# Optimization experiments

Measured on AMD Instinct MI355X. Metric: run time of the kernel, lower is better.

Reference implementation:

```python
import jax, jax.numpy as jnp
import numpy as np

B = 2048

def _conv(x, w, b, stride):
    y = jax.lax.conv_general_dilated(x, w, (stride, stride), 'VALID',
                                     dimension_numbers=('NCHW', 'OIHW', 'NCHW'))
    return y + b[None, :, None, None]

def _local_conv(x, w, b):
    # w: (Ho, Wo, Co, Ci, kh, kw), b: (Ho, Wo, Co); stride 1, valid
    Ho, Wo, Co, Ci, kh, kw = w.shape
    # patches: (B, Ci, kh*kw, Ho, Wo) -- sliding windows, small fixed loop over kernel taps
    patches = jnp.stack([x[:, :, i:i + Ho, j:j + Wo]
                         for i in range(kh) for j in range(kw)], axis=2)
    wf = w.reshape(Ho, Wo, Co, Ci, kh * kw)
    y = jnp.einsum('bcphw,hwocp->bohw', patches, wf)
    return y + jnp.transpose(b, (2, 0, 1))[None]

def setup_inputs() -> dict:
    key = jax.random.key(0)
    ks = jax.random.split(key, 18)
    s = 0.05
    inp = {
        'x': jax.random.normal(ks[0], (B, 5, 60, 60), dtype=jnp.float32),
        'info': jax.random.normal(ks[1], (B, 8), dtype=jnp.float32),
        'w1': jax.random.normal(ks[2], (32, 5, 3, 3), dtype=jnp.float32) * s,
        'b1': jnp.zeros((32,), dtype=jnp.float32),
        'w2a': jax.random.normal(ks[3], (64, 32, 3, 3), dtype=jnp.float32) * s,
        'b2a': jnp.zeros((64,), dtype=jnp.float32),
        'w2b': jax.random.normal(ks[4], (64, 64, 3, 3), dtype=jnp.float32) * s,
        'b2b': jnp.zeros((64,), dtype=jnp.float32),
        'lw3': jax.random.normal(ks[5], (9, 9, 64, 64, 5, 5), dtype=jnp.float32) * s,
        'lb3': jnp.zeros((9, 9, 64), dtype=jnp.float32),
        'lw4': jax.random.normal(ks[6], (5, 5, 64, 64, 5, 5), dtype=jnp.float32) * s,
        'lb4': jnp.zeros((5, 5, 64), dtype=jnp.float32),
        'lw5': jax.random.normal(ks[7], (3, 3, 64, 64, 3, 3), dtype=jnp.float32) * s,
        'lb5': jnp.zeros((3, 3, 64), dtype=jnp.float32),
        'hw': jax.random.normal(ks[8], (2, 584), dtype=jnp.float32) * s,
        'hb': jnp.zeros((2,), dtype=jnp.float32),
    }
    return inp

def reference(x, info, w1, b1, w2a, b2a, w2b, b2b, lw3, lb3, lw4, lb4, lw5, lb5, hw, hb):
    h = jnp.tanh(_conv(x, w1, b1, 2))            # (B,32,29,29)
    h = jnp.tanh(_conv(h, w2a, b2a, 1))          # (B,64,27,27)
    h = jnp.tanh(_conv(h, w2b, b2b, 2))          # (B,64,13,13)
    h = jnp.tanh(_local_conv(h, lw3, lb3))       # (B,64,9,9)
    h = jnp.tanh(_local_conv(h, lw4, lb4))       # (B,64,5,5)
    h = jnp.tanh(_local_conv(h, lw5, lb5))       # (B,64,3,3)
    h = h.reshape(h.shape[0], -1)                # (B,576)
    h = jnp.concatenate([h, info], axis=1)       # (B,584)
    logits = h @ hw.T + hb                       # (B,2)
    return jax.nn.softmax(logits, axis=1)
```

## Files before the change

kernel.cpp:

```cpp
#include <hip/hip_runtime.h>
#include <stdint.h>

#define THREADS 256

typedef short bf16x8 __attribute__((ext_vector_type(8)));
typedef float f32x4 __attribute__((ext_vector_type(4)));
typedef unsigned uint2_ __attribute__((ext_vector_type(2)));
typedef unsigned short ushort4_ __attribute__((ext_vector_type(4)));

#define GPTR(x) ((const __attribute__((address_space(1))) void*)(x))
#define LPTR(x) ((__attribute__((address_space(3))) void*)(x))

__device__ __forceinline__ unsigned short f2bf(float v) {
  unsigned u = __builtin_bit_cast(unsigned, v);
  u = (u + 0x7fff + ((u >> 16) & 1)) >> 16;
  return (unsigned short)u;
}
__device__ __forceinline__ float bf2f(unsigned short h) {
  return __builtin_bit_cast(float, (unsigned)h << 16);
}
__device__ __forceinline__ float fast_tanh(float x) {
  return 1.f - 2.f / (__expf(2.f * x) + 1.f);
}

__global__ void pack_w1t(const float* __restrict__ w1, float* __restrict__ w1t) {
  int idx = blockIdx.x * THREADS + threadIdx.x;
  if (idx >= 45 * 32) return;
  int t = idx >> 5, co = idx & 31;
  w1t[t * 32 + co] = w1[co * 45 + t];
}

__global__ void __launch_bounds__(256) conv1_direct(
    const float* __restrict__ x, const float* __restrict__ w1t,
    const float* __restrict__ bias, unsigned short* __restrict__ out, int Bc,
    int bstart) {
  constexpr int CI = 5, CO = 32, IH = 60, IW = 60, OH = 29, OW = 29;
  constexpr int RPB = 2, NRB = 15;

  __shared__ float xs[CI * 5 * 60];

  const int tid = threadIdx.x;
  const int b = blockIdx.x / NRB;
  const int qb = blockIdx.x % NRB;
  const int oh0 = qb * RPB;
  const int rows = min(RPB, OH - oh0);
  const int ih0 = oh0 * 2;
  const int ihn = rows * 2 + 1;

  const float* xp = x + (size_t)(bstart + b) * (CI * IH * IW);

  const int nf4 = CI * ihn * 15;
  for (int i = tid; i < nf4; i += 256) {
    int col = i % 15;
    int row = i / 15;
    int ci = row / ihn, r = row % ihn;
    ((float4*)xs)[row * 15 + col] = ((const float4*)xp)[(ci * IH + ih0 + r) * 15 + col];
  }
  __syncthreads();

  const int lane = tid & 63;
  const int wu = __builtin_amdgcn_readfirstlane(tid >> 6);
  if (lane >= rows * OW) return;
  const int r = lane / OW, c = lane % OW;
  const int base = (r * 2) * 60 + c * 2;
  const int cstr = ihn * 60;

  float acc[8];
#pragma unroll
  for (int j = 0; j < 8; j++) acc[j] = bias[wu * 8 + j];

#pragma unroll
  for (int ci = 0; ci < CI; ci++)
#pragma unroll
    for (int kh = 0; kh < 3; kh++)
#pragma unroll
      for (int kw = 0; kw < 3; kw++) {
        const float v = xs[ci * cstr + base + kh * 60 + kw];
        const float* wt = w1t + ((ci * 3 + kh) * 3 + kw) * 32 + wu * 8;
#pragma unroll
        for (int j = 0; j < 8; j++) acc[j] = fmaf(v, wt[j], acc[j]);
      }

  const int p = (oh0 + r) * OW + c;
  bf16x8 o;
#pragma unroll
  for (int j = 0; j < 8; j++) o[j] = (short)f2bf(fast_tanh(acc[j]));
  *(bf16x8*)(out + ((size_t)p * Bc + b) * CO + wu * 8) = o;
}

template <int CI, int KS>
__global__ void __launch_bounds__(THREADS) pack_w(const float* __restrict__ w,
                                                  unsigned short* __restrict__ wp,
                                                  int npos) {
  constexpr int K = CI * KS * KS;
  constexpr int S = K / 32;
  int idx = blockIdx.x * THREADS + threadIdx.x;
  int total = npos * S * 2048;
  if (idx >= total) return;
  int e = idx & 7;
  int lane = (idx >> 3) & 63;
  int mt = (idx >> 9) & 3;
  int rest = idx >> 11;
  int s = rest % S, pos = rest / S;
  int co = mt * 16 + (lane & 15);
  int k = s * 32 + (lane >> 4) * 8 + e;
  int tap = k / CI, ci = k % CI;
  int kh = tap / KS, kw = tap % KS;
  float v = w[((((size_t)pos * 64 + co) * CI + ci) * KS + kh) * KS + kw];
  wp[idx] = f2bf(v);
}

template <int CI, int IH, int IW, int OH, int OW, int KS, int ST, bool LOCAL, int BT>
__global__ void __launch_bounds__(256) conv_mfma(
    const unsigned short* __restrict__ X, const unsigned short* __restrict__ Wp,
    const float* __restrict__ bias, unsigned short* __restrict__ Y, int Bc) {
  constexpr int S = CI * KS * KS / 32;
  constexpr int NPOS = OH * OW;
  constexpr int BW = BT / 64;
  constexpr int CW = 4 / BW;
  constexpr int MT = 4 / CW;

  __shared__ unsigned short aT[2][2048];

  const int tid = threadIdx.x;
  const int lane = tid & 63;
  const int wu = tid >> 6;
  const int n = lane & 15, g = lane >> 4;
  const int bw = wu % BW, cw = wu / BW;

  int wg = blockIdx.x;
  {
    const int nwg = gridDim.x;
    const int q = nwg >> 3, rr = nwg & 7;
    const int xcd = wg & 7, l = wg >> 3;
    wg = (xcd < rr ? xcd * (q + 1) : rr * (q + 1) + (xcd - rr) * q) + l;
  }
  const int pos = wg % NPOS;
  const int btile = wg / NPOS;
  const int oh = pos / OW, ow = pos % OW;
  const int b0 = btile * BT + bw * 64;

  const unsigned short* Wpp = Wp + (LOCAL ? (size_t)pos * (S * 2048) : 0);

  f32x4 acc[MT][4] = {};

  const int bA = b0 + n;

  __builtin_amdgcn_global_load_lds(GPTR(Wpp + tid * 8), LPTR(&aT[0][tid * 8]), 16, 0, 0);

  int buf = 0;
  for (int s = 0; s < S; s++) {
    __syncthreads();
    if (s + 1 < S)
      __builtin_amdgcn_global_load_lds(GPTR(Wpp + (s + 1) * 2048 + tid * 8),
                                       LPTR(&aT[buf ^ 1][tid * 8]), 16, 0, 0);

    const int tap = (s * 32) / CI;
    const int ci0 = (s * 32) % CI + g * 8;
    const int kh = tap / KS, kw = tap % KS;
    const int pin = (oh * ST + kh) * IW + (ow * ST + kw);
    const unsigned short* xb = X + ((size_t)pin * Bc + bA) * CI + ci0;

    bf16x8 bfr[4];
#pragma unroll
    for (int j = 0; j < 4; j++) bfr[j] = *(const bf16x8*)(xb + j * 16 * CI);

    bf16x8 af[MT];
#pragma unroll
    for (int mt = 0; mt < MT; mt++)
      af[mt] = *(const bf16x8*)(&aT[buf][((cw * MT + mt) * 64 + lane) * 8]);

#pragma unroll
    for (int mt = 0; mt < MT; mt++)
#pragma unroll
      for (int j = 0; j < 4; j++)
        acc[mt][j] =
            __builtin_amdgcn_mfma_f32_16x16x32_bf16(af[mt], bfr[j], acc[mt][j], 0, 0, 0);
    buf ^= 1;
  }

#pragma unroll
  for (int mt = 0; mt < MT; mt++) {
#pragma unroll
    for (int j = 0; j < 4; j++) {
      unsigned short o[4];
#pragma unroll
      for (int r = 0; r < 4; r++) {
        const int co = (cw * MT + mt) * 16 + g * 4 + r;
        const float bv = LOCAL ? bias[pos * 64 + co] : bias[co];
        o[r] = f2bf(fast_tanh(acc[mt][j][r] + bv));
      }
      const int b = b0 + j * 16 + n;
      uint2_ pk;
      pk[0] = (unsigned)o[0] | ((unsigned)o[1] << 16);
      pk[1] = (unsigned)o[2] | ((unsigned)o[3] << 16);
      *(uint2_*)(Y + ((size_t)pos * Bc + b) * 64 + (cw * MT + mt) * 16 + g * 4) = pk;
    }
  }
}

__global__ void head_k(const unsigned short* __restrict__ h5,
                       const float* __restrict__ info, const float* __restrict__ hw,
                       const float* __restrict__ hb, float* __restrict__ out, int Bc,
                       int bstart) {
  int b = blockIdx.x * THREADS + threadIdx.x;
  if (b >= Bc) return;
  float l0 = hb[0], l1 = hb[1];
  for (int pos = 0; pos < 9; pos++) {
#pragma unroll
    for (int cb = 0; cb < 8; cb++) {
      bf16x8 v8 = *(const bf16x8*)(h5 + ((size_t)pos * Bc + b) * 64 + cb * 8);
#pragma unroll
      for (int j = 0; j < 8; j++) {
        float v = bf2f((unsigned short)v8[j]);
        int f = (cb * 8 + j) * 9 + pos;
        l0 = fmaf(v, hw[f], l0);
        l1 = fmaf(v, hw[584 + f], l1);
      }
    }
  }
#pragma unroll
  for (int k = 0; k < 8; k++) {
    float v = info[(size_t)(bstart + b) * 8 + k];
    l0 = fmaf(v, hw[576 + k], l0);
    l1 = fmaf(v, hw[584 + 576 + k], l1);
  }
  float m = fmaxf(l0, l1);
  float e0 = __expf(l0 - m), e1 = __expf(l1 - m);
  float s = e0 + e1;
  out[(size_t)(bstart + b) * 2 + 0] = e0 / s;
  out[(size_t)(bstart + b) * 2 + 1] = e1 / s;
}


extern "C" void kernel_launch(void* const* d_in, const int* in_sizes, int n_in,
                              void* d_out, int out_size, void* d_ws, size_t ws_size,
                              hipStream_t stream) {
  const float* x = (const float*)d_in[0];
  const float* info = (const float*)d_in[1];
  const float* w1 = (const float*)d_in[2];
  const float* b1 = (const float*)d_in[3];
  const float* w2a = (const float*)d_in[4];
  const float* b2a = (const float*)d_in[5];
  const float* w2b = (const float*)d_in[6];
  const float* b2b = (const float*)d_in[7];
  const float* lw3 = (const float*)d_in[8];
  const float* lb3 = (const float*)d_in[9];
  const float* lw4 = (const float*)d_in[10];
  const float* lb4 = (const float*)d_in[11];
  const float* lw5 = (const float*)d_in[12];
  const float* lb5 = (const float*)d_in[13];
  const float* hw = (const float*)d_in[14];
  const float* hb = (const float*)d_in[15];
  float* out = (float*)d_out;

  const int B = in_sizes[0] / 18000;

  const size_t SZ2A = 9ull * 2048, SZ2B = 18ull * 2048, SZ3 = 81ull * 50 * 2048,
               SZ4 = 25ull * 50 * 2048, SZ5 = 9ull * 18 * 2048;
  unsigned short* wp2a = (unsigned short*)d_ws;
  unsigned short* wp2b = wp2a + SZ2A;
  unsigned short* wp3 = wp2b + SZ2B;
  unsigned short* wp4 = wp3 + SZ3;
  unsigned short* wp5 = wp4 + SZ4;
  size_t wp_bytes = (SZ2A + SZ2B + SZ3 + SZ4 + SZ5) * 2;
  wp_bytes = (wp_bytes + 255) & ~(size_t)255;
  float* w1t = (float*)((char*)d_ws + wp_bytes);
  size_t w1t_bytes = ((45 * 32 * 4) + 255) & ~(size_t)255;

  const size_t per_sample = 53824 + 93312;
  int Bc = B;
  while (Bc > 256 && wp_bytes + w1t_bytes + (size_t)Bc * per_sample + 4096 > ws_size)
    Bc >>= 1;

  unsigned short* bufA = (unsigned short*)((char*)d_ws + wp_bytes + w1t_bytes);
  unsigned short* bufB =
      (unsigned short*)((char*)d_ws + wp_bytes + w1t_bytes + (size_t)Bc * 53824);

  hipLaunchKernelGGL(pack_w1t, dim3(6), dim3(THREADS), 0, stream, w1, w1t);
  hipLaunchKernelGGL((pack_w<32, 3>), dim3((SZ2A + 255) / 256), dim3(THREADS), 0, stream,
                     w2a, wp2a, 1);
  hipLaunchKernelGGL((pack_w<64, 3>), dim3((SZ2B + 255) / 256), dim3(THREADS), 0, stream,
                     w2b, wp2b, 1);
  hipLaunchKernelGGL((pack_w<64, 5>), dim3((SZ3 + 255) / 256), dim3(THREADS), 0, stream,
                     lw3, wp3, 81);
  hipLaunchKernelGGL((pack_w<64, 5>), dim3((SZ4 + 255) / 256), dim3(THREADS), 0, stream,
                     lw4, wp4, 25);
  hipLaunchKernelGGL((pack_w<64, 3>), dim3((SZ5 + 255) / 256), dim3(THREADS), 0, stream,
                     lw5, wp5, 9);

  const int nchunks = B / Bc;
  for (int c = 0; c < nchunks; c++) {
    const int bstart = c * Bc;

    hipLaunchKernelGGL(conv1_direct, dim3(Bc * 15), dim3(256), 0, stream, x, w1t, b1,
                       bufA, Bc, bstart);
    hipLaunchKernelGGL((conv_mfma<32, 29, 29, 27, 27, 3, 1, false, 256>),
                       dim3(729 * (Bc / 256)), dim3(256), 0, stream, bufA, wp2a, b2a,
                       bufB, Bc);
    hipLaunchKernelGGL((conv_mfma<64, 27, 27, 13, 13, 3, 2, false, 256>),
                       dim3(169 * (Bc / 256)), dim3(256), 0, stream, bufB, wp2b, b2b,
                       bufA, Bc);
    hipLaunchKernelGGL((conv_mfma<64, 13, 13, 9, 9, 5, 1, true, 256>),
                       dim3(81 * (Bc / 256)), dim3(256), 0, stream, bufA, wp3, lb3, bufB,
                       Bc);
    hipLaunchKernelGGL((conv_mfma<64, 9, 9, 5, 5, 5, 1, true, 128>),
                       dim3(25 * (Bc / 128)), dim3(256), 0, stream, bufB, wp4, lb4, bufA,
                       Bc);
    hipLaunchKernelGGL((conv_mfma<64, 5, 5, 3, 3, 3, 1, true, 64>),
                       dim3(9 * (Bc / 64)), dim3(256), 0, stream, bufA, wp5, lb5, bufB,
                       Bc);
    hipLaunchKernelGGL(head_k, dim3((Bc + THREADS - 1) / THREADS), dim3(THREADS), 0,
                       stream, bufB, info, hw, hb, out, Bc, bstart);
  }
}
```

Measured before the change: 567.0 us.

## Preload full conv weights into LDS, read local-conv weights directly from global

For the shared-weight convolutions, each block now loads the entire packed weight tensor into dynamic LDS once, up front, instead of double-buffering one slice per K-step. This removes the per-iteration barrier. The locally-connected layers skip LDS and have each wave read its weight fragments straight from global memory, and the K loop is unrolled by two. The batch chunk is also capped at 1024, which changes the number of passes and the working-set size. The risks are larger LDS use (up to 72KB), which may lower occupancy, and uncoalesced or redundant global weight reads in the local layers.

```diff
diff --git a/kernel.cpp b/kernel.cpp
--- a/kernel.cpp
+++ b/kernel.cpp
@@ -120,7 +120,7 @@
   constexpr int CW = 4 / BW;
   constexpr int MT = 4 / CW;
 
-  __shared__ unsigned short aT[2][2048];
+  extern __shared__ unsigned short wlds[];
 
   const int tid = threadIdx.x;
   const int lane = tid & 63;
@@ -142,19 +142,18 @@
 
   const unsigned short* Wpp = Wp + (LOCAL ? (size_t)pos * (S * 2048) : 0);
 
+  if (!LOCAL) {
+    for (int i = tid; i < S * 256; i += 256)
+      __builtin_amdgcn_global_load_lds(GPTR(Wpp + (size_t)i * 8),
+                                       LPTR(wlds + (size_t)i * 8), 16, 0, 0);
+    __syncthreads();
+  }
+
   f32x4 acc[MT][4] = {};
-
   const int bA = b0 + n;
 
-  __builtin_amdgcn_global_load_lds(GPTR(Wpp + tid * 8), LPTR(&aT[0][tid * 8]), 16, 0, 0);
-
-  int buf = 0;
+#pragma unroll 2
   for (int s = 0; s < S; s++) {
-    __syncthreads();
-    if (s + 1 < S)
-      __builtin_amdgcn_global_load_lds(GPTR(Wpp + (s + 1) * 2048 + tid * 8),
-                                       LPTR(&aT[buf ^ 1][tid * 8]), 16, 0, 0);
-
     const int tap = (s * 32) / CI;
     const int ci0 = (s * 32) % CI + g * 8;
     const int kh = tap / KS, kw = tap % KS;
@@ -167,8 +166,13 @@
 
     bf16x8 af[MT];
 #pragma unroll
-    for (int mt = 0; mt < MT; mt++)
-      af[mt] = *(const bf16x8*)(&aT[buf][((cw * MT + mt) * 64 + lane) * 8]);
+    for (int mt = 0; mt < MT; mt++) {
+      const int t = cw * MT + mt;
+      if (LOCAL)
+        af[mt] = *(const bf16x8*)(Wpp + ((size_t)((s * 4 + t) * 64 + lane) << 3));
+      else
+        af[mt] = *(const bf16x8*)(wlds + ((size_t)((s * 4 + t) * 64 + lane) << 3));
+    }
 
 #pragma unroll
     for (int mt = 0; mt < MT; mt++)
@@ -176,7 +180,6 @@
       for (int j = 0; j < 4; j++)
         acc[mt][j] =
             __builtin_amdgcn_mfma_f32_16x16x32_bf16(af[mt], bfr[j], acc[mt][j], 0, 0, 0);
-    buf ^= 1;
   }
 
 #pragma unroll
@@ -270,6 +273,7 @@
 
   const size_t per_sample = 53824 + 93312;
   int Bc = B;
+  if (Bc > 1024) Bc = 1024;
   while (Bc > 256 && wp_bytes + w1t_bytes + (size_t)Bc * per_sample + 4096 > ws_size)
     Bc >>= 1;
 
@@ -296,11 +300,11 @@
     hipLaunchKernelGGL(conv1_direct, dim3(Bc * 15), dim3(256), 0, stream, x, w1t, b1,
                        bufA, Bc, bstart);
     hipLaunchKernelGGL((conv_mfma<32, 29, 29, 27, 27, 3, 1, false, 256>),
-                       dim3(729 * (Bc / 256)), dim3(256), 0, stream, bufA, wp2a, b2a,
-                       bufB, Bc);
+                       dim3(729 * (Bc / 256)), dim3(256), 9 * 4096, stream, bufA, wp2a,
+                       b2a, bufB, Bc);
     hipLaunchKernelGGL((conv_mfma<64, 27, 27, 13, 13, 3, 2, false, 256>),
-                       dim3(169 * (Bc / 256)), dim3(256), 0, stream, bufB, wp2b, b2b,
-                       bufA, Bc);
+                       dim3(169 * (Bc / 256)), dim3(256), 18 * 4096, stream, bufB, wp2b,
+                       b2b, bufA, Bc);
     hipLaunchKernelGGL((conv_mfma<64, 13, 13, 9, 9, 5, 1, true, 256>),
                        dim3(81 * (Bc / 256)), dim3(256), 0, stream, bufA, wp3, lb3, bufB,
                        Bc);
```

Result: slower. 642.7 us (+13.4%).

## Keep dense conv weights in registers and read local-conv weights directly

Applied to the files above, without the earlier changes.

Adds a dense conv kernel that loads all weight fragments into registers once per block and sweeps a whole output row. The conv2b layer is split into two K-halves that pass a float32 partial accumulator through global memory, so the register-resident weights fit. The local-conv kernel drops the LDS double buffer and barrier and reads weights straight from global memory, with wider batch tiles (512 threads for layer 3). The intent is to remove the per-step weight staging and syncs and to reuse weights across positions. In exchange it adds the fp32 partial-sum round trip, higher register pressure and a larger workspace requirement.

```diff
diff --git a/kernel.cpp b/kernel.cpp
--- a/kernel.cpp
+++ b/kernel.cpp
@@ -8,9 +8,6 @@
 typedef unsigned uint2_ __attribute__((ext_vector_type(2)));
 typedef unsigned short ushort4_ __attribute__((ext_vector_type(4)));
 
-#define GPTR(x) ((const __attribute__((address_space(1))) void*)(x))
-#define LPTR(x) ((__attribute__((address_space(3))) void*)(x))
-
 __device__ __forceinline__ unsigned short f2bf(float v) {
   unsigned u = __builtin_bit_cast(unsigned, v);
   u = (u + 0x7fff + ((u >> 16) & 1)) >> 16;
@@ -21,6 +18,12 @@
 }
 __device__ __forceinline__ float fast_tanh(float x) {
   return 1.f - 2.f / (__expf(2.f * x) + 1.f);
+}
+
+__device__ __forceinline__ int xcd_swizzle(int wg, int nwg) {
+  const int q = nwg >> 3, rr = nwg & 7;
+  const int xcd = wg & 7, l = wg >> 3;
+  return (xcd < rr ? xcd * (q + 1) : rr * (q + 1) + (xcd - rr) * q) + l;
 }
 
 __global__ void pack_w1t(const float* __restrict__ w1, float* __restrict__ w1t) {
@@ -110,17 +113,88 @@
   wp[idx] = f2bf(v);
 }
 
-template <int CI, int IH, int IW, int OH, int OW, int KS, int ST, bool LOCAL, int BT>
-__global__ void __launch_bounds__(256) conv_mfma(
+template <int CI, int IH, int IW, int OH, int OW, int KS, int ST, int SP, int SOFF,
+          int MODE>
+__global__ void __launch_bounds__(256) conv_dense_reg(
+    const unsigned short* __restrict__ X, const unsigned short* __restrict__ Wp,
+    const float* __restrict__ bias, unsigned short* __restrict__ Y,
+    float* __restrict__ ACC, int Bc) {
+  const int tid = threadIdx.x;
+  const int lane = tid & 63;
+  const int wu = tid >> 6;
+  const int n = lane & 15, g = lane >> 4;
+
+  const int nbt = Bc >> 6;
+  int wg = xcd_swizzle(blockIdx.x, gridDim.x);
+  const int oh = wg / nbt;
+  const int bt = wg - oh * nbt;
+  const int bA = bt * 64 + wu * 16 + n;
+
+  bf16x8 af[SP][4];
+#pragma unroll
+  for (int s = 0; s < SP; s++)
+#pragma unroll
+    for (int mt = 0; mt < 4; mt++)
+      af[s][mt] = *(const bf16x8*)(Wp + ((size_t)(((SOFF + s) * 4 + mt) * 64 + lane) << 3));
+
+  f32x4 bv[4];
+  if (MODE != 0) {
+#pragma unroll
+    for (int mt = 0; mt < 4; mt++) bv[mt] = *(const f32x4*)(bias + mt * 16 + g * 4);
+  }
+
+  for (int ow = 0; ow < OW; ow++) {
+    const int pos = oh * OW + ow;
+    f32x4 acc[4];
+    if (MODE == 1) {
+#pragma unroll
+      for (int mt = 0; mt < 4; mt++)
+        acc[mt] = *(const f32x4*)(ACC + ((size_t)pos * Bc + bA) * 64 + mt * 16 + g * 4);
+    } else {
+#pragma unroll
+      for (int mt = 0; mt < 4; mt++) acc[mt] = (f32x4){0.f, 0.f, 0.f, 0.f};
+    }
+
+#pragma unroll
+    for (int s = 0; s < SP; s++) {
+      const int sg = SOFF + s;
+      const int tap = (sg * 32) / CI;
+      const int ci0 = (sg * 32) % CI + g * 8;
+      const int kh = tap / KS, kw = tap % KS;
+      const int pin = (oh * ST + kh) * IW + (ow * ST + kw);
+      const bf16x8 bfr = *(const bf16x8*)(X + ((size_t)pin * Bc + bA) * CI + ci0);
+#pragma unroll
+      for (int mt = 0; mt < 4; mt++)
+        acc[mt] = __builtin_amdgcn_mfma_f32_16x16x32_bf16(af[s][mt], bfr, acc[mt], 0, 0, 0);
+    }
+
+    if (MODE == 0) {
+#pragma unroll
+      for (int mt = 0; mt < 4; mt++)
+        *(f32x4*)(ACC + ((size_t)pos * Bc + bA) * 64 + mt * 16 + g * 4) = acc[mt];
+    } else {
+#pragma unroll
+      for (int mt = 0; mt < 4; mt++) {
+        unsigned short o[4];
+#pragma unroll
+        for (int r = 0; r < 4; r++) o[r] = f2bf(fast_tanh(acc[mt][r] + bv[mt][r]));
+        uint2_ pk;
+        pk[0] = (unsigned)o[0] | ((unsigned)o[1] << 16);
+        pk[1] = (unsigned)o[2] | ((unsigned)o[3] << 16);
+        *(uint2_*)(Y + ((size_t)pos * Bc + bA) * 64 + mt * 16 + g * 4) = pk;
+      }
+    }
+  }
+}
+
+template <int CI, int IH, int IW, int OH, int OW, int KS, int ST, int NW, int BW>
+__global__ void __launch_bounds__(NW * 64) conv_local(
     const unsigned short* __restrict__ X, const unsigned short* __restrict__ Wp,
     const float* __restrict__ bias, unsigned short* __restrict__ Y, int Bc) {
   constexpr int S = CI * KS * KS / 32;
   constexpr int NPOS = OH * OW;
-  constexpr int BW = BT / 64;
-  constexpr int CW = 4 / BW;
+  constexpr int CW = NW / BW;
   constexpr int MT = 4 / CW;
-
-  __shared__ unsigned short aT[2][2048];
 
   const int tid = threadIdx.x;
   const int lane = tid & 63;
@@ -128,33 +202,19 @@
   const int n = lane & 15, g = lane >> 4;
   const int bw = wu % BW, cw = wu / BW;
 
-  int wg = blockIdx.x;
-  {
-    const int nwg = gridDim.x;
-    const int q = nwg >> 3, rr = nwg & 7;
-    const int xcd = wg & 7, l = wg >> 3;
-    wg = (xcd < rr ? xcd * (q + 1) : rr * (q + 1) + (xcd - rr) * q) + l;
-  }
+  int wg = xcd_swizzle(blockIdx.x, gridDim.x);
   const int pos = wg % NPOS;
   const int btile = wg / NPOS;
   const int oh = pos / OW, ow = pos % OW;
-  const int b0 = btile * BT + bw * 64;
-
-  const unsigned short* Wpp = Wp + (LOCAL ? (size_t)pos * (S * 2048) : 0);
+  const int b0 = btile * (BW * 64) + bw * 64;
+  const int bA = b0 + n;
+
+  const unsigned short* Wpp = Wp + (size_t)pos * (S * 2048);
 
   f32x4 acc[MT][4] = {};
 
-  const int bA = b0 + n;
-
-  __builtin_amdgcn_global_load_lds(GPTR(Wpp + tid * 8), LPTR(&aT[0][tid * 8]), 16, 0, 0);
-
-  int buf = 0;
+#pragma unroll 2
   for (int s = 0; s < S; s++) {
-    __syncthreads();
-    if (s + 1 < S)
-      __builtin_amdgcn_global_load_lds(GPTR(Wpp + (s + 1) * 2048 + tid * 8),
-                                       LPTR(&aT[buf ^ 1][tid * 8]), 16, 0, 0);
-
     const int tap = (s * 32) / CI;
     const int ci0 = (s * 32) % CI + g * 8;
     const int kh = tap / KS, kw = tap % KS;
@@ -168,7 +228,8 @@
     bf16x8 af[MT];
 #pragma unroll
     for (int mt = 0; mt < MT; mt++)
-      af[mt] = *(const bf16x8*)(&aT[buf][((cw * MT + mt) * 64 + lane) * 8]);
+      af[mt] =
+          *(const bf16x8*)(Wpp + ((size_t)((s * 4 + cw * MT + mt) * 64 + lane) << 3));
 
 #pragma unroll
     for (int mt = 0; mt < MT; mt++)
@@ -176,7 +237,6 @@
       for (int j = 0; j < 4; j++)
         acc[mt][j] =
             __builtin_amdgcn_mfma_f32_16x16x32_bf16(af[mt], bfr[j], acc[mt][j], 0, 0, 0);
-    buf ^= 1;
   }
 
 #pragma unroll
@@ -187,8 +247,7 @@
 #pragma unroll
       for (int r = 0; r < 4; r++) {
         const int co = (cw * MT + mt) * 16 + g * 4 + r;
-        const float bv = LOCAL ? bias[pos * 64 + co] : bias[co];
-        o[r] = f2bf(fast_tanh(acc[mt][j][r] + bv));
+        o[r] = f2bf(fast_tanh(acc[mt][j][r] + bias[pos * 64 + co]));
       }
       const int b = b0 + j * 16 + n;
       uint2_ pk;
@@ -268,14 +327,16 @@
   float* w1t = (float*)((char*)d_ws + wp_bytes);
   size_t w1t_bytes = ((45 * 32 * 4) + 255) & ~(size_t)255;
 
-  const size_t per_sample = 53824 + 93312;
+  const size_t PSA = 53824, PSB = 93312, PSC = 43264;
+  const size_t per_sample = PSA + PSB + PSC;
   int Bc = B;
-  while (Bc > 256 && wp_bytes + w1t_bytes + (size_t)Bc * per_sample + 4096 > ws_size)
+  while (Bc > 512 && wp_bytes + w1t_bytes + (size_t)Bc * per_sample + 4096 > ws_size)
     Bc >>= 1;
 
-  unsigned short* bufA = (unsigned short*)((char*)d_ws + wp_bytes + w1t_bytes);
-  unsigned short* bufB =
-      (unsigned short*)((char*)d_ws + wp_bytes + w1t_bytes + (size_t)Bc * 53824);
+  char* base = (char*)d_ws + wp_bytes + w1t_bytes;
+  unsigned short* bufA = (unsigned short*)base;
+  unsigned short* bufB = (unsigned short*)(base + (size_t)Bc * PSA);
+  float* acc2b = (float*)(base + (size_t)Bc * (PSA + PSB));
 
   hipLaunchKernelGGL(pack_w1t, dim3(6), dim3(THREADS), 0, stream, w1, w1t);
   hipLaunchKernelGGL((pack_w<32, 3>), dim3((SZ2A + 255) / 256), dim3(THREADS), 0, stream,
@@ -295,19 +356,22 @@
 
     hipLaunchKernelGGL(conv1_direct, dim3(Bc * 15), dim3(256), 0, stream, x, w1t, b1,
                        bufA, Bc, bstart);
-    hipLaunchKernelGGL((conv_mfma<32, 29, 29, 27, 27, 3, 1, false, 256>),
-                       dim3(729 * (Bc / 256)), dim3(256), 0, stream, bufA, wp2a, b2a,
-                       bufB, Bc);
-    hipLaunchKernelGGL((conv_mfma<64, 27, 27, 13, 13, 3, 2, false, 256>),
-                       dim3(169 * (Bc / 256)), dim3(256), 0, stream, bufB, wp2b, b2b,
-                       bufA, Bc);
-    hipLaunchKernelGGL((conv_mfma<64, 13, 13, 9, 9, 5, 1, true, 256>),
-                       dim3(81 * (Bc / 256)), dim3(256), 0, stream, bufA, wp3, lb3, bufB,
+    hipLaunchKernelGGL((conv_dense_reg<32, 29, 29, 27, 27, 3, 1, 9, 0, 2>),
+                       dim3(27 * (Bc / 64)), dim3(256), 0, stream, bufA, wp2a, b2a, bufB,
+                       (float*)nullptr, Bc);
+    hipLaunchKernelGGL((conv_dense_reg<64, 27, 27, 13, 13, 3, 2, 9, 0, 0>),
+                       dim3(13 * (Bc / 64)), dim3(256), 0, stream, bufB, wp2b, b2b,
+                       (unsigned short*)nullptr, acc2b, Bc);
+    hipLaunchKernelGGL((conv_dense_reg<64, 27, 27, 13, 13, 3, 2, 9, 9, 1>),
+                       dim3(13 * (Bc / 64)), dim3(256), 0, stream, bufB, wp2b, b2b, bufA,
+                       acc2b, Bc);
+    hipLaunchKernelGGL((conv_local<64, 13, 13, 9, 9, 5, 1, 8, 8>),
+                       dim3(81 * (Bc / 512)), dim3(512), 0, stream, bufA, wp3, lb3, bufB,
                        Bc);
-    hipLaunchKernelGGL((conv_mfma<64, 9, 9, 5, 5, 5, 1, true, 128>),
-                       dim3(25 * (Bc / 128)), dim3(256), 0, stream, bufB, wp4, lb4, bufA,
+    hipLaunchKernelGGL((conv_local<64, 9, 9, 5, 5, 5, 1, 4, 4>),
+                       dim3(25 * (Bc / 256)), dim3(256), 0, stream, bufB, wp4, lb4, bufA,
                        Bc);
-    hipLaunchKernelGGL((conv_mfma<64, 5, 5, 3, 3, 3, 1, true, 64>),
+    hipLaunchKernelGGL((conv_local<64, 5, 5, 3, 3, 3, 1, 4, 1>),
                        dim3(9 * (Bc / 64)), dim3(256), 0, stream, bufA, wp5, lb5, bufB,
                        Bc);
     hipLaunchKernelGGL(head_k, dim3((Bc + THREADS - 1) / THREADS), dim3(THREADS), 0,
```

Result: slower. 726.8 us (+28.2%).

## Load conv weights directly from global, drop LDS staging, reorder local tile mapping

Applied to the files above, without the earlier changes.

Removes the LDS double-buffered weight staging and its per-step barrier in the MFMA conv kernel, so each wave reads its weight fragments straight from global memory (relying on L1/L2 caching). For locally connected layers, the workgroup index is remapped so that consecutive workgroups share a position and its weights, which is meant to improve weight reuse in cache. The template parameter changes from a batch tile to a wave count, and the loop is unrolled by two. The cost is redundant global weight loads across waves and no explicit prefetch.

```diff
diff --git a/kernel.cpp b/kernel.cpp
--- a/kernel.cpp
+++ b/kernel.cpp
@@ -6,10 +6,6 @@
 typedef short bf16x8 __attribute__((ext_vector_type(8)));
 typedef float f32x4 __attribute__((ext_vector_type(4)));
 typedef unsigned uint2_ __attribute__((ext_vector_type(2)));
-typedef unsigned short ushort4_ __attribute__((ext_vector_type(4)));
-
-#define GPTR(x) ((const __attribute__((address_space(1))) void*)(x))
-#define LPTR(x) ((__attribute__((address_space(3))) void*)(x))
 
 __device__ __forceinline__ unsigned short f2bf(float v) {
   unsigned u = __builtin_bit_cast(unsigned, v);
@@ -21,6 +17,12 @@
 }
 __device__ __forceinline__ float fast_tanh(float x) {
   return 1.f - 2.f / (__expf(2.f * x) + 1.f);
+}
+
+__device__ __forceinline__ int xcd_swizzle(int wg, int nwg) {
+  const int q = nwg >> 3, rr = nwg & 7;
+  const int xcd = wg & 7, l = wg >> 3;
+  return (xcd < rr ? xcd * (q + 1) : rr * (q + 1) + (xcd - rr) * q) + l;
 }
 
 __global__ void pack_w1t(const float* __restrict__ w1, float* __restrict__ w1t) {
@@ -110,17 +112,14 @@
   wp[idx] = f2bf(v);
 }
 
-template <int CI, int IH, int IW, int OH, int OW, int KS, int ST, bool LOCAL, int BT>
+template <int CI, int IH, int IW, int OH, int OW, int KS, int ST, bool LOCAL, int BW>
 __global__ void __launch_bounds__(256) conv_mfma(
     const unsigned short* __restrict__ X, const unsigned short* __restrict__ Wp,
     const float* __restrict__ bias, unsigned short* __restrict__ Y, int Bc) {
   constexpr int S = CI * KS * KS / 32;
   constexpr int NPOS = OH * OW;
-  constexpr int BW = BT / 64;
   constexpr int CW = 4 / BW;
   constexpr int MT = 4 / CW;
-
-  __shared__ unsigned short aT[2][2048];
 
   const int tid = threadIdx.x;
   const int lane = tid & 63;
@@ -128,33 +127,26 @@
   const int n = lane & 15, g = lane >> 4;
   const int bw = wu % BW, cw = wu / BW;
 
-  int wg = blockIdx.x;
-  {
-    const int nwg = gridDim.x;
-    const int q = nwg >> 3, rr = nwg & 7;
-    const int xcd = wg & 7, l = wg >> 3;
-    wg = (xcd < rr ? xcd * (q + 1) : rr * (q + 1) + (xcd - rr) * q) + l;
-  }
-  const int pos = wg % NPOS;
-  const int btile = wg / NPOS;
+  const int nbt = Bc / (BW * 64);
+  int wg = xcd_swizzle(blockIdx.x, gridDim.x);
+  int pos, btile;
+  if (LOCAL) {
+    btile = wg % nbt;
+    pos = wg / nbt;
+  } else {
+    pos = wg % NPOS;
+    btile = wg / NPOS;
+  }
   const int oh = pos / OW, ow = pos % OW;
-  const int b0 = btile * BT + bw * 64;
+  const int b0 = btile * (BW * 64) + bw * 64;
+  const int bA = b0 + n;
 
   const unsigned short* Wpp = Wp + (LOCAL ? (size_t)pos * (S * 2048) : 0);
 
   f32x4 acc[MT][4] = {};
 
-  const int bA = b0 + n;
-
-  __builtin_amdgcn_global_load_lds(GPTR(Wpp + tid * 8), LPTR(&aT[0][tid * 8]), 16, 0, 0);
-
-  int buf = 0;
+#pragma unroll 2
   for (int s = 0; s < S; s++) {
-    __syncthreads();
-    if (s + 1 < S)
-      __builtin_amdgcn_global_load_lds(GPTR(Wpp + (s + 1) * 2048 + tid * 8),
-                                       LPTR(&aT[buf ^ 1][tid * 8]), 16, 0, 0);
-
     const int tap = (s * 32) / CI;
     const int ci0 = (s * 32) % CI + g * 8;
     const int kh = tap / KS, kw = tap % KS;
@@ -168,7 +160,8 @@
     bf16x8 af[MT];
 #pragma unroll
     for (int mt = 0; mt < MT; mt++)
-      af[mt] = *(const bf16x8*)(&aT[buf][((cw * MT + mt) * 64 + lane) * 8]);
+      af[mt] =
+          *(const bf16x8*)(Wpp + ((size_t)((s * 4 + cw * MT + mt) * 64 + lane) << 3));
 
 #pragma unroll
     for (int mt = 0; mt < MT; mt++)
@@ -176,7 +169,6 @@
       for (int j = 0; j < 4; j++)
         acc[mt][j] =
             __builtin_amdgcn_mfma_f32_16x16x32_bf16(af[mt], bfr[j], acc[mt][j], 0, 0, 0);
-    buf ^= 1;
   }
 
 #pragma unroll
@@ -187,8 +179,8 @@
 #pragma unroll
       for (int r = 0; r < 4; r++) {
         const int co = (cw * MT + mt) * 16 + g * 4 + r;
-        const float bv = LOCAL ? bias[pos * 64 + co] : bias[co];
-        o[r] = f2bf(fast_tanh(acc[mt][j][r] + bv));
+        o[r] = f2bf(fast_tanh(acc[mt][j][r] +
+                              (LOCAL ? bias[pos * 64 + co] : bias[co])));
       }
       const int b = b0 + j * 16 + n;
       uint2_ pk;
@@ -268,14 +260,15 @@
   float* w1t = (float*)((char*)d_ws + wp_bytes);
   size_t w1t_bytes = ((45 * 32 * 4) + 255) & ~(size_t)255;
 
-  const size_t per_sample = 53824 + 93312;
+  const size_t PSA = 53824, PSB = 93312;
+  const size_t per_sample = PSA + PSB;
   int Bc = B;
   while (Bc > 256 && wp_bytes + w1t_bytes + (size_t)Bc * per_sample + 4096 > ws_size)
     Bc >>= 1;
 
-  unsigned short* bufA = (unsigned short*)((char*)d_ws + wp_bytes + w1t_bytes);
-  unsigned short* bufB =
-      (unsigned short*)((char*)d_ws + wp_bytes + w1t_bytes + (size_t)Bc * 53824);
+  char* base = (char*)d_ws + wp_bytes + w1t_bytes;
+  unsigned short* bufA = (unsigned short*)base;
+  unsigned short* bufB = (unsigned short*)(base + (size_t)Bc * PSA);
 
   hipLaunchKernelGGL(pack_w1t, dim3(6), dim3(THREADS), 0, stream, w1, w1t);
   hipLaunchKernelGGL((pack_w<32, 3>), dim3((SZ2A + 255) / 256), dim3(THREADS), 0, stream,
@@ -295,19 +288,19 @@
 
     hipLaunchKernelGGL(conv1_direct, dim3(Bc * 15), dim3(256), 0, stream, x, w1t, b1,
                        bufA, Bc, bstart);
-    hipLaunchKernelGGL((conv_mfma<32, 29, 29, 27, 27, 3, 1, false, 256>),
+    hipLaunchKernelGGL((conv_mfma<32, 29, 29, 27, 27, 3, 1, false, 4>),
                        dim3(729 * (Bc / 256)), dim3(256), 0, stream, bufA, wp2a, b2a,
                        bufB, Bc);
-    hipLaunchKernelGGL((conv_mfma<64, 27, 27, 13, 13, 3, 2, false, 256>),
+    hipLaunchKernelGGL((conv_mfma<64, 27, 27, 13, 13, 3, 2, false, 4>),
                        dim3(169 * (Bc / 256)), dim3(256), 0, stream, bufB, wp2b, b2b,
                        bufA, Bc);
-    hipLaunchKernelGGL((conv_mfma<64, 13, 13, 9, 9, 5, 1, true, 256>),
+    hipLaunchKernelGGL((conv_mfma<64, 13, 13, 9, 9, 5, 1, true, 4>),
                        dim3(81 * (Bc / 256)), dim3(256), 0, stream, bufA, wp3, lb3, bufB,
                        Bc);
-    hipLaunchKernelGGL((conv_mfma<64, 9, 9, 5, 5, 5, 1, true, 128>),
+    hipLaunchKernelGGL((conv_mfma<64, 9, 9, 5, 5, 5, 1, true, 2>),
                        dim3(25 * (Bc / 128)), dim3(256), 0, stream, bufB, wp4, lb4, bufA,
                        Bc);
-    hipLaunchKernelGGL((conv_mfma<64, 5, 5, 3, 3, 3, 1, true, 64>),
+    hipLaunchKernelGGL((conv_mfma<64, 5, 5, 3, 3, 3, 1, true, 1>),
                        dim3(9 * (Bc / 64)), dim3(256), 0, stream, bufA, wp5, lb5, bufB,
                        Bc);
     hipLaunchKernelGGL(head_k, dim3((Bc + THREADS - 1) / THREADS), dim3(THREADS), 0,
```

New measurement: 640.7 us. 1.13x slower.
